# Kernel tuning notes

Measured on AMD Instinct MI355X. Metric: run time of the kernel, lower is better.

The kernel has to match this reference:

```python
import jax, jax.numpy as jnp
import numpy as np


def setup_inputs() -> dict:
    key = jax.random.key(0)
    k1, k2, k3, k4 = jax.random.split(key, 4)
    B, N, d_in, d_out = 8, 2048, 256, 256
    x = jax.random.normal(k1, (B, N, d_in), dtype=jnp.float32)
    adj_hat = jax.random.uniform(k2, (B, N, N), dtype=jnp.float32)
    W = jax.random.normal(k3, (d_out, d_in), dtype=jnp.float32) * (1.0 / np.sqrt(d_in))
    b = jax.random.normal(k4, (d_out,), dtype=jnp.float32) * 0.01
    return {"x": x, "adj_hat": adj_hat, "W": W, "b": b}


def reference(x, adj_hat, W, b):
    # Degrees from adj = adj_hat - I (i.e. without self loops): row sum minus diagonal.
    N = adj_hat.shape[1]
    diag = jnp.diagonal(adj_hat, axis1=-2, axis2=-1)          # [B, N]
    d = adj_hat.sum(axis=-1) - diag                           # [B, N]
    d_inv_sqrt = jnp.power(d, -0.5)                           # [B, N]
    # dad = D^-1/2 @ adj_hat @ D^-1/2  ==  d_i * a_ij * d_j (elementwise broadcast)
    dad = d_inv_sqrt[:, :, None] * adj_hat * d_inv_sqrt[:, None, :]  # [B, N, N]
    h = jnp.einsum('bnd,od->bno', x, W) + b                   # projection [B, N, d_out]
    return jnp.einsum('bnm,bmo->bno', dad, h)                 # [B, N, d_out]
```

## Files before the change

kernel.cpp:

```cpp
#include <hip/hip_runtime.h>
#include <hip/hip_bf16.h>


#define BATCH 8
#define NN    2048
#define DIN   256
#define DOUT  256
#define RTOT  (BATCH * NN)
#define HP    (RTOT + 32)

typedef short  bf16x8  __attribute__((ext_vector_type(8)));
typedef short  short4v __attribute__((ext_vector_type(4)));
typedef float  f32x4   __attribute__((ext_vector_type(4)));

__device__ __forceinline__ short f2bf(float f) {
    union { float f; unsigned u; } v; v.f = f;
    unsigned r = v.u + 0x7fffu + ((v.u >> 16) & 1u);
    return (short)(r >> 16);
}

__device__ __forceinline__ void gl_lds16(const unsigned short* g, unsigned short* l) {
    __builtin_amdgcn_global_load_lds(
        (const __attribute__((address_space(1))) unsigned int*)g,
        (__attribute__((address_space(3))) unsigned int*)l, 16, 0, 0);
}

__global__ __launch_bounds__(256) void k_deg_proj(const float* __restrict__ adj,
                                                  const float* __restrict__ x,
                                                  const float* __restrict__ W,
                                                  const float* __restrict__ bias,
                                                  float* __restrict__ dis,
                                                  unsigned short* __restrict__ hT) {
    const int tid = threadIdx.x;

    if (blockIdx.x < 256) {
        const int bid = blockIdx.x;
        const int mt  = bid >> 7;
        const int nt  = bid & 127;
        const int w = tid >> 6, lane = tid & 63;
        const int wr = w >> 1, wc = w & 1;
        const int l16 = lane & 15, quad = lane >> 4;

        __shared__ short As[128][32];
        __shared__ short Bs[128][32];

        f32x4 acc[4][4];
#pragma unroll
        for (int i = 0; i < 4; i++)
#pragma unroll
            for (int j = 0; j < 4; j++) acc[i][j] = (f32x4){0.f, 0.f, 0.f, 0.f};

        const float4* Wf4 = (const float4*)(W + (size_t)mt * 128 * DIN);
        const float4* Xf4 = (const float4*)(x + (size_t)nt * 128 * DIN);

        for (int kk = 0; kk < DIN / 32; kk++) {
            const int k0 = kk * 32;
            __syncthreads();
#pragma unroll
            for (int it = 0; it < 4; it++) {
                int idx = tid + it * 256;
                int r = idx >> 3, c = idx & 7;
                float4 va = Wf4[(size_t)r * (DIN / 4) + (k0 >> 2) + c];
                float4 vb = Xf4[(size_t)r * (DIN / 4) + (k0 >> 2) + c];
                short4v sa = { f2bf(va.x), f2bf(va.y), f2bf(va.z), f2bf(va.w) };
                short4v sb = { f2bf(vb.x), f2bf(vb.y), f2bf(vb.z), f2bf(vb.w) };
                *(short4v*)&As[r][c * 4] = sa;
                *(short4v*)&Bs[r][c * 4] = sb;
            }
            __syncthreads();
            bf16x8 af[4], bfv[4];
#pragma unroll
            for (int i = 0; i < 4; i++) af[i]  = *(bf16x8*)&As[wr * 64 + i * 16 + l16][quad * 8];
#pragma unroll
            for (int j = 0; j < 4; j++) bfv[j] = *(bf16x8*)&Bs[wc * 64 + j * 16 + l16][quad * 8];
#pragma unroll
            for (int i = 0; i < 4; i++)
#pragma unroll
                for (int j = 0; j < 4; j++)
                    acc[i][j] = __builtin_amdgcn_mfma_f32_16x16x32_bf16(af[i], bfv[j], acc[i][j], 0, 0, 0);
        }

#pragma unroll
        for (int i = 0; i < 4; i++) {
            const int orow_base = mt * 128 + wr * 64 + i * 16 + quad * 4;
#pragma unroll
            for (int r = 0; r < 4; r++) {
                const int orow = orow_base + r;
                const float bb = bias[orow];
#pragma unroll
                for (int j = 0; j < 4; j++) {
                    const int col = nt * 128 + wc * 64 + j * 16 + l16;
                    float v = acc[i][j][r] + bb;
                    hT[(size_t)orow * HP + col] = (unsigned short)f2bf(v);
                }
            }
        }
    } else {
        const int row = blockIdx.x - 256;
        const int n = row & (NN - 1);
        const float4* rp4 = (const float4*)(adj + (size_t)row * NN);

        float s = 0.f;
#pragma unroll
        for (int i = 0; i < 2; i++) {
            float4 v = rp4[tid + i * 256];
            s += (v.x + v.y) + (v.z + v.w);
        }
#pragma unroll
        for (int off = 32; off; off >>= 1) s += __shfl_down(s, off);
        __shared__ float red[4];
        if ((tid & 63) == 0) red[tid >> 6] = s;
        __syncthreads();
        if (tid == 0) {
            float tot  = (red[0] + red[1]) + (red[2] + red[3]);
            float diag = ((const float*)rp4)[n];
            dis[row]   = rsqrtf(tot - diag);
        }
    }
}

__global__ __launch_bounds__(256, 2) void k_main(const float* __restrict__ adj,
                                                 const unsigned short* __restrict__ hT,
                                                 const float* __restrict__ dis,
                                                 float* __restrict__ out) {
    const int bx    = blockIdx.x;
    const int b     = bx & 7;
    const int mtile = (bx >> 3) & 31;
    const int ctile = bx >> 8;
    const int n0    = mtile * 64;
    const int tid  = threadIdx.x;
    const int w    = tid >> 6, lane = tid & 63;
    const int l16  = lane & 15, quad = lane >> 4;
    const int lr   = lane >> 2;
    const int lc   = (lane & 3) * 8;

    __shared__ short As[4][64][32];
    __shared__ short Bs[4][128][32];

    const float* disb = dis + (size_t)b * NN;
    const float4* agf4 = (const float4*)(adj + (size_t)(b * NN + n0 + w * 16 + lr) * NN + lc);
    const unsigned short* bgp0 = hT + (size_t)(ctile * 128 + w * 32 + lr) * HP + b * NN + lc;
    const unsigned short* bgp1 = bgp0 + (size_t)16 * HP;

    f32x4 acc[4][2];
#pragma unroll
    for (int i = 0; i < 4; i++)
#pragma unroll
        for (int j = 0; j < 2; j++) acc[i][j] = (f32x4){0.f, 0.f, 0.f, 0.f};

    for (int g = 0; g < NN / 128; g++) {
#pragma unroll
        for (int s = 0; s < 4; s++) {
            const int ko = g * 128 + s * 32;
            gl_lds16(bgp0 + ko, (unsigned short*)&Bs[s][w * 32][0]);
            gl_lds16(bgp1 + ko, (unsigned short*)&Bs[s][w * 32 + 16][0]);
        }
        float4 av0[4], av1[4];
#pragma unroll
        for (int s = 0; s < 4; s++) {
            av0[s] = agf4[g * 32 + s * 8];
            av1[s] = agf4[g * 32 + s * 8 + 1];
        }
#pragma unroll
        for (int s = 0; s < 4; s++) {
            const float* dp = disb + g * 128 + s * 32 + lc;
            float4 dv0 = *(const float4*)dp;
            float4 dv1 = *(const float4*)(dp + 4);
            bf16x8 pk = { f2bf(av0[s].x * dv0.x), f2bf(av0[s].y * dv0.y),
                          f2bf(av0[s].z * dv0.z), f2bf(av0[s].w * dv0.w),
                          f2bf(av1[s].x * dv1.x), f2bf(av1[s].y * dv1.y),
                          f2bf(av1[s].z * dv1.z), f2bf(av1[s].w * dv1.w) };
            *(bf16x8*)&As[s][w * 16 + lr][lc] = pk;
        }
        __syncthreads();
#pragma unroll
        for (int s = 0; s < 4; s++) {
            bf16x8 af[4], bfv[2];
#pragma unroll
            for (int i = 0; i < 4; i++) af[i]  = *(bf16x8*)&As[s][i * 16 + l16][quad * 8];
#pragma unroll
            for (int j = 0; j < 2; j++) bfv[j] = *(bf16x8*)&Bs[s][w * 32 + j * 16 + l16][quad * 8];
#pragma unroll
            for (int i = 0; i < 4; i++)
#pragma unroll
                for (int j = 0; j < 2; j++)
                    acc[i][j] = __builtin_amdgcn_mfma_f32_16x16x32_bf16(af[i], bfv[j], acc[i][j], 0, 0, 0);
        }
        __syncthreads();
    }

#pragma unroll
    for (int i = 0; i < 4; i++) {
#pragma unroll
        for (int r = 0; r < 4; r++) {
            const int nrow = n0 + i * 16 + quad * 4 + r;
            const float dn = disb[nrow];
#pragma unroll
            for (int j = 0; j < 2; j++) {
                const int ocol = ctile * 128 + w * 32 + j * 16 + l16;
                out[((size_t)b * NN + nrow) * DOUT + ocol] = dn * acc[i][j][r];
            }
        }
    }
}

extern "C" void kernel_launch(void* const* d_in, const int* in_sizes, int n_in,
                              void* d_out, int out_size, void* d_ws, size_t ws_size,
                              hipStream_t stream) {
    const float* x    = (const float*)d_in[0];
    const float* adj  = (const float*)d_in[1];
    const float* W    = (const float*)d_in[2];
    const float* bias = (const float*)d_in[3];
    float* out = (float*)d_out;

    float* dis = (float*)d_ws;
    unsigned short* hT  = (unsigned short*)((char*)d_ws + 65536);

    k_deg_proj<<<256 + RTOT, 256, 0, stream>>>(adj, x, W, bias, dis, hT);
    k_main<<<512, 256, 0, stream>>>(adj, hT, dis, out);
}
```

Measured before the change: 244.6 us.

## Retile main GEMM to 32-row tiles covering full output width

The main kernel now gives each block 32 adjacency rows and all 256 output columns, where before it had 64 rows and half the columns. Each adjacency element is therefore read from global memory once instead of twice, which cuts the dominant fp32 adjacency traffic. In exchange each block loads the full 256-column hT slice per k-step, so hT traffic and LDS footprint double and MFMA work per A fragment changes. The adjacency loads are also rearranged so consecutive threads read consecutive float4s along a row.

```diff
diff --git a/kernel.cpp b/kernel.cpp
--- a/kernel.cpp
+++ b/kernel.cpp
@@ -125,79 +125,75 @@
                                                  float* __restrict__ out) {
     const int bx    = blockIdx.x;
     const int b     = bx & 7;
-    const int mtile = (bx >> 3) & 31;
-    const int ctile = bx >> 8;
-    const int n0    = mtile * 64;
+    const int mtile = bx >> 3;
+    const int n0    = mtile * 32;
     const int tid  = threadIdx.x;
     const int w    = tid >> 6, lane = tid & 63;
     const int l16  = lane & 15, quad = lane >> 4;
     const int lr   = lane >> 2;
     const int lc   = (lane & 3) * 8;
-
-    __shared__ short As[4][64][32];
-    __shared__ short Bs[4][128][32];
+    const int ar   = tid >> 3;
+    const int ac   = (tid & 7) * 4;
+
+    __shared__ short As[4][32][32];
+    __shared__ short Bs[4][256][32];
 
     const float* disb = dis + (size_t)b * NN;
-    const float4* agf4 = (const float4*)(adj + (size_t)(b * NN + n0 + w * 16 + lr) * NN + lc);
-    const unsigned short* bgp0 = hT + (size_t)(ctile * 128 + w * 32 + lr) * HP + b * NN + lc;
-    const unsigned short* bgp1 = bgp0 + (size_t)16 * HP;
-
-    f32x4 acc[4][2];
-#pragma unroll
-    for (int i = 0; i < 4; i++)
-#pragma unroll
-        for (int j = 0; j < 2; j++) acc[i][j] = (f32x4){0.f, 0.f, 0.f, 0.f};
+    const float4* agf4 = (const float4*)(adj + (size_t)(b * NN + n0 + ar) * NN);
+    const unsigned short* bgp = hT + (size_t)(w * 16 + lr) * HP + b * NN + lc;
+
+    f32x4 acc[2][4];
+#pragma unroll
+    for (int i = 0; i < 2; i++)
+#pragma unroll
+        for (int j = 0; j < 4; j++) acc[i][j] = (f32x4){0.f, 0.f, 0.f, 0.f};
 
     for (int g = 0; g < NN / 128; g++) {
 #pragma unroll
         for (int s = 0; s < 4; s++) {
             const int ko = g * 128 + s * 32;
-            gl_lds16(bgp0 + ko, (unsigned short*)&Bs[s][w * 32][0]);
-            gl_lds16(bgp1 + ko, (unsigned short*)&Bs[s][w * 32 + 16][0]);
-        }
-        float4 av0[4], av1[4];
+#pragma unroll
+            for (int i = 0; i < 4; i++)
+                gl_lds16(bgp + (size_t)i * 64 * HP + ko,
+                         (unsigned short*)&Bs[s][w * 16 + i * 64][0]);
+        }
+        float4 av[4], dv[4];
+#pragma unroll
+        for (int s = 0; s < 4; s++) av[s] = agf4[g * 32 + s * 8 + (tid & 7)];
+#pragma unroll
+        for (int s = 0; s < 4; s++) dv[s] = *(const float4*)(disb + g * 128 + s * 32 + ac);
 #pragma unroll
         for (int s = 0; s < 4; s++) {
-            av0[s] = agf4[g * 32 + s * 8];
-            av1[s] = agf4[g * 32 + s * 8 + 1];
-        }
+            short4v pk = { f2bf(av[s].x * dv[s].x), f2bf(av[s].y * dv[s].y),
+                           f2bf(av[s].z * dv[s].z), f2bf(av[s].w * dv[s].w) };
+            *(short4v*)&As[s][ar][ac] = pk;
+        }
+        __syncthreads();
 #pragma unroll
         for (int s = 0; s < 4; s++) {
-            const float* dp = disb + g * 128 + s * 32 + lc;
-            float4 dv0 = *(const float4*)dp;
-            float4 dv1 = *(const float4*)(dp + 4);
-            bf16x8 pk = { f2bf(av0[s].x * dv0.x), f2bf(av0[s].y * dv0.y),
-                          f2bf(av0[s].z * dv0.z), f2bf(av0[s].w * dv0.w),
-                          f2bf(av1[s].x * dv1.x), f2bf(av1[s].y * dv1.y),
-                          f2bf(av1[s].z * dv1.z), f2bf(av1[s].w * dv1.w) };
-            *(bf16x8*)&As[s][w * 16 + lr][lc] = pk;
-        }
-        __syncthreads();
-#pragma unroll
-        for (int s = 0; s < 4; s++) {
-            bf16x8 af[4], bfv[2];
-#pragma unroll
-            for (int i = 0; i < 4; i++) af[i]  = *(bf16x8*)&As[s][i * 16 + l16][quad * 8];
-#pragma unroll
-            for (int j = 0; j < 2; j++) bfv[j] = *(bf16x8*)&Bs[s][w * 32 + j * 16 + l16][quad * 8];
-#pragma unroll
-            for (int i = 0; i < 4; i++)
-#pragma unroll
-                for (int j = 0; j < 2; j++)
+            bf16x8 af[2], bfv[4];
+#pragma unroll
+            for (int i = 0; i < 2; i++) af[i]  = *(bf16x8*)&As[s][i * 16 + l16][quad * 8];
+#pragma unroll
+            for (int j = 0; j < 4; j++) bfv[j] = *(bf16x8*)&Bs[s][w * 64 + j * 16 + l16][quad * 8];
+#pragma unroll
+            for (int i = 0; i < 2; i++)
+#pragma unroll
+                for (int j = 0; j < 4; j++)
                     acc[i][j] = __builtin_amdgcn_mfma_f32_16x16x32_bf16(af[i], bfv[j], acc[i][j], 0, 0, 0);
         }
         __syncthreads();
     }
 
 #pragma unroll
-    for (int i = 0; i < 4; i++) {
+    for (int i = 0; i < 2; i++) {
 #pragma unroll
         for (int r = 0; r < 4; r++) {
             const int nrow = n0 + i * 16 + quad * 4 + r;
             const float dn = disb[nrow];
 #pragma unroll
-            for (int j = 0; j < 2; j++) {
-                const int ocol = ctile * 128 + w * 32 + j * 16 + l16;
+            for (int j = 0; j < 4; j++) {
+                const int ocol = w * 64 + j * 16 + l16;
                 out[((size_t)b * NN + nrow) * DOUT + ocol] = dn * acc[i][j][r];
             }
         }
```

Result: slower. 256.7 us (+4.9%).
